# Kernel tuning notes

Hardware: AMD Instinct MI355X
Metric: run time of the kernel (lower is better)

Reference implementation:

```python
import jax, jax.numpy as jnp
import numpy as np

EPS = 1e-5


def layernorm(h, w, b):
    mu = jnp.mean(h, axis=-1, keepdims=True)
    var = jnp.mean((h - mu) ** 2, axis=-1, keepdims=True)
    return (h - mu) * jax.lax.rsqrt(var + EPS) * w + b


def pos_encoding(length, d_model):
    # PE(pos,2i)=sin(pos/10000^(2i/d)), PE(pos,2i+1)=cos(...)
    pos = jnp.arange(length, dtype=jnp.float32)[:, None]
    div = jnp.exp(jnp.arange(0, d_model, 2, dtype=jnp.float32) * (-np.log(10000.0) / d_model))
    pe = jnp.zeros((length, d_model), dtype=jnp.float32)
    pe = pe.at[:, 0::2].set(jnp.sin(pos * div))
    pe = pe.at[:, 1::2].set(jnp.cos(pos * div))
    return pe


def setup_inputs() -> dict:
    key = jax.random.key(0)
    ks = jax.random.split(key, 4)
    B, N, K, S = 4, 256, 128, 256
    return {
        "x": jax.random.normal(ks[0], (B, N, K, S), dtype=jnp.float32),
        "ln1_w": jnp.ones((N,), jnp.float32),
        "ln1_b": jnp.zeros((N,), jnp.float32),
        "q_w": jax.random.normal(ks[1], (N, N), jnp.float32) * 0.02,
        "q_b": jnp.zeros((N,), jnp.float32),
        "k_w": jax.random.normal(ks[2], (N, N), jnp.float32) * 0.02,
        "k_b": jnp.zeros((N,), jnp.float32),
        "v_w": jax.random.normal(ks[3], (N, N), jnp.float32) * 0.02,
        "v_b": jnp.zeros((N,), jnp.float32),
        "ln2_w": jnp.ones((N,), jnp.float32),
        "ln2_b": jnp.zeros((N,), jnp.float32),
    }


def reference(x, ln1_w, ln1_b, q_w, q_b, k_w, k_b, v_w, v_b, ln2_w, ln2_b):
    B, N, K, S = x.shape
    scale = 1.0 / np.sqrt(N)  # dim_k == in_channels
    # (B, N, K, S) -> (B*K, S, N)
    h = x.transpose(0, 2, 3, 1).reshape(B * K, S, N)
    h = layernorm(h, ln1_w, ln1_b) + pos_encoding(S, N)[None]
    res = h
    Q = h @ q_w.T + q_b
    Kt = h @ k_w.T + k_b
    V = h @ v_w.T + v_b
    # Faithful to source: softmax FIRST, then multiply by 1/sqrt(dim_k)
    att = jax.nn.softmax(jnp.einsum('bqd,bkd->bqk', Q, Kt), axis=-1) * scale
    h = res + jnp.einsum('bqk,bkd->bqd', att, V)  # dropout = identity (eval)
    h = layernorm(h, ln2_w, ln2_b)
    return h.reshape(B, K, S, N).transpose(0, 3, 1, 2) + x
```

## Files before the change

### kernel.cpp

```cpp
#include <hip/hip_runtime.h>


using short8  = __attribute__((ext_vector_type(8))) short;
using floatx4 = __attribute__((ext_vector_type(4))) float;

#define KSX 32768

__device__ __forceinline__ ushort f2bf(float f) {
    uint u = __float_as_uint(f);
    u += 0x7fffu + ((u >> 16) & 1u);
    return (ushort)(u >> 16);
}
__device__ __forceinline__ float bf2f(ushort h) {
    return __uint_as_float(((uint)h) << 16);
}

__global__ __launch_bounds__(256) void prep_kernel(
    const float* __restrict__ qw, const float* __restrict__ kw,
    const float* __restrict__ vw,
    float* __restrict__ pe, ushort* __restrict__ wpack)
{
    int tid = blockIdx.x * 256 + threadIdx.x;
    if (tid < 65536) {
        int n = tid >> 8, s = tid & 255;
        float d = expf(-0.03597789207803196f * (float)(n & ~1));
        float a = d * (float)s;
        pe[tid] = (n & 1) ? cosf(a) : sinf(a);
    } else {
        int id = tid - 65536;
        int wsel = id >> 16;
        int e = id & 65535;
        const float* w = (wsel == 0) ? qw : ((wsel == 1) ? kw : vw);
        int j    = e & 7;
        int lane = (e >> 3) & 63;
        int fr   = e >> 9;
        int nt   = fr & 15;
        int mc   = fr >> 4;
        int row  = (lane & 15) + 16 * nt;
        int col  = 8 * (lane >> 4) + j + 32 * mc;
        wpack[wsel * 65536 + e] = f2bf(w[row * 256 + col]);
    }
}

__global__ __launch_bounds__(512, 2) void attn_kernel(
    const float* __restrict__ x,
    const float* __restrict__ ln1w, const float* __restrict__ ln1b,
    const float* __restrict__ qbias, const float* __restrict__ kbias,
    const float* __restrict__ vbias,
    const float* __restrict__ ln2w, const float* __restrict__ ln2b,
    const float* __restrict__ pe, const ushort* __restrict__ wpack,
    float* __restrict__ out)
{
    __shared__ ushort ldsA[128 * 256];
    __shared__ ushort ldsB[128 * 256];
    __shared__ ushort bounce[8 * 512];
    __shared__ float  smallbuf[1792];
    __shared__ float  stats[512];

    const int tid = threadIdx.x;
    const int wid = tid >> 6;
    const int l   = tid & 63;
    const int c   = l & 15;
    const int g   = l >> 4;

    const int bk   = blockIdx.x;
    const int base = (bk >> 7) * (256 * KSX) + (bk & 127) * 256;
    const float* xb = x + base;
    float* ob = out + base;

    const short8* wq8 = (const short8*)(wpack);
    const short8* wk8 = (const short8*)(wpack + 65536);
    const short8* wv8 = (const short8*)(wpack + 131072);

    {
        int i = tid;
        smallbuf[i] = (i < 256) ? ln1w[i] : ln1b[i - 256];
        i = tid + 512;
        smallbuf[i] = (i < 768) ? ln2w[i - 512] : ln2b[i - 768];
        i = tid + 1024;
        smallbuf[i] = (i < 1280) ? qbias[i - 1024] : kbias[i - 1280];
        if (tid < 256) smallbuf[tid + 1536] = vbias[tid];
    }
    __syncthreads();

    ushort* bnc = bounce + (wid << 9);

    short8 Hfrag[2][8];
    #pragma unroll
    for (int t = 0; t < 2; ++t) {
        const int s = 16 * wid + 128 * t + c;
        float sum = 0.f, ssq = 0.f;
        #pragma unroll
        for (int mc = 0; mc < 8; ++mc) {
            short8 hp;
            #pragma unroll
            for (int j = 0; j < 8; ++j) {
                int m = 32 * mc + 8 * g + j;
                float v = xb[m * KSX + s];
                ushort hb = f2bf(v);
                hp[j] = (short)hb;
                float vb = bf2f(hb);
                sum += vb; ssq += vb * vb;
            }
            Hfrag[t][mc] = hp;
        }
        sum += __shfl_xor(sum, 16); ssq += __shfl_xor(ssq, 16);
        sum += __shfl_xor(sum, 32); ssq += __shfl_xor(ssq, 32);
        float mu   = sum * (1.f / 256.f);
        float var  = ssq * (1.f / 256.f) - mu * mu;
        float rstd = rsqrtf(var + 1e-5f);
        #pragma unroll
        for (int mc = 0; mc < 8; ++mc) {
            short8 hp = Hfrag[t][mc];
            #pragma unroll
            for (int j = 0; j < 8; ++j) {
                int m = 32 * mc + 8 * g + j;
                float v = bf2f((ushort)hp[j]);
                float h = (v - mu) * rstd * smallbuf[m] + smallbuf[256 + m]
                          + pe[m * 256 + s];
                hp[j] = (short)f2bf(h);
            }
            Hfrag[t][mc] = hp;
        }
        if (g == 0) { stats[2 * s] = mu; stats[2 * s + 1] = rstd; }
    }

    short8 Qfrag[2][8];
    #pragma unroll
    for (int t = 0; t < 2; ++t) {
        #pragma unroll
        for (int nc = 0; nc < 8; ++nc) {
            floatx4 acc0 = {0.f, 0.f, 0.f, 0.f};
            floatx4 acc1 = {0.f, 0.f, 0.f, 0.f};
            #pragma unroll
            for (int mc = 0; mc < 8; ++mc) {
                short8 a  = Hfrag[t][mc];
                short8 b0 = wq8[(mc * 16 + 2 * nc) * 64 + l];
                short8 b1 = wq8[(mc * 16 + 2 * nc + 1) * 64 + l];
                acc0 = __builtin_amdgcn_mfma_f32_16x16x32_bf16(a, b0, acc0, 0, 0, 0);
                acc1 = __builtin_amdgcn_mfma_f32_16x16x32_bf16(a, b1, acc1, 0, 0, 0);
            }
            #pragma unroll
            for (int e = 0; e < 2; ++e) {
                floatx4 acc = e ? acc1 : acc0;
                float bias = smallbuf[1024 + 16 * (2 * nc + e) + c];
                #pragma unroll
                for (int r = 0; r < 4; ++r) {
                    int row = 4 * g + r;
                    int col = 16 * e + c;
                    bnc[row * 32 + (col ^ ((row & 3) << 3))] = f2bf(acc[r] + bias);
                }
            }
            Qfrag[t][nc] = *(const short8*)&bnc[c * 32 + ((8 * g) ^ ((c & 3) << 3))];
        }
    }

    #pragma unroll
    for (int hf = 0; hf < 2; ++hf) {
        ushort* reg = hf ? ldsB : ldsA;
        #pragma unroll
        for (int nt = 0; nt < 16; ++nt) {
            floatx4 acc = {0.f, 0.f, 0.f, 0.f};
            #pragma unroll
            for (int mc = 0; mc < 8; ++mc)
                acc = __builtin_amdgcn_mfma_f32_16x16x32_bf16(
                    Hfrag[hf][mc], wk8[(mc * 16 + nt) * 64 + l], acc, 0, 0, 0);
            int n = 16 * nt + c;
            float bias = smallbuf[1280 + n];
            #pragma unroll
            for (int r = 0; r < 4; ++r) {
                int kkl = 16 * wid + 4 * g + r;
                reg[kkl * 256 + (n ^ ((kkl & 7) << 3))] = f2bf(acc[r] + bias);
            }
        }
    }
    __syncthreads();

    uint  Spack[2][4][8];
    float mloc[8];
    #pragma unroll
    for (int i = 0; i < 8; ++i) mloc[i] = -3.0e38f;

    #pragma unroll
    for (int ct = 0; ct < 16; ++ct) {
        const ushort* reg = (ct < 8) ? ldsA : ldsB;
        int kt = ct & 7;
        short8 bfr[8];
        #pragma unroll
        for (int mt = 0; mt < 8; ++mt) {
            int kkl = c + 16 * kt;
            int n0  = 32 * mt + 8 * g;
            bfr[mt] = *(const short8*)&reg[kkl * 256 + (n0 ^ ((kkl & 7) << 3))];
        }
        #pragma unroll
        for (int t = 0; t < 2; ++t) {
            floatx4 acc = {0.f, 0.f, 0.f, 0.f};
            #pragma unroll
            for (int mt = 0; mt < 8; ++mt)
                acc = __builtin_amdgcn_mfma_f32_16x16x32_bf16(
                    Qfrag[t][mt], bfr[mt], acc, 0, 0, 0);
            #pragma unroll
            for (int r = 0; r < 4; ++r) {
                float v = acc[r];
                mloc[t * 4 + r] = fmaxf(mloc[t * 4 + r], v);
                ushort hb = f2bf(v);
                if (ct & 1)
                    Spack[t][r][ct >> 1] = (Spack[t][r][ct >> 1] & 0xffffu) | ((uint)hb << 16);
                else
                    Spack[t][r][ct >> 1] = hb;
            }
        }
    }

    #pragma unroll
    for (int i = 0; i < 8; ++i) {
        mloc[i] = fmaxf(mloc[i], __shfl_xor(mloc[i], 1));
        mloc[i] = fmaxf(mloc[i], __shfl_xor(mloc[i], 2));
        mloc[i] = fmaxf(mloc[i], __shfl_xor(mloc[i], 4));
        mloc[i] = fmaxf(mloc[i], __shfl_xor(mloc[i], 8));
    }
    float lsum[8];
    #pragma unroll
    for (int i = 0; i < 8; ++i) lsum[i] = 0.f;
    #pragma unroll
    for (int t = 0; t < 2; ++t) {
        #pragma unroll
        for (int r = 0; r < 4; ++r) {
            float m = mloc[t * 4 + r];
            #pragma unroll
            for (int d0 = 0; d0 < 8; ++d0) {
                uint d = Spack[t][r][d0];
                float e0 = __expf(bf2f((ushort)(d & 0xffffu)) - m);
                float e1 = __expf(bf2f((ushort)(d >> 16)) - m);
                lsum[t * 4 + r] += e0 + e1;
                Spack[t][r][d0] = (uint)f2bf(e0) | ((uint)f2bf(e1) << 16);
            }
        }
    }
    #pragma unroll
    for (int i = 0; i < 8; ++i) {
        lsum[i] += __shfl_xor(lsum[i], 1);
        lsum[i] += __shfl_xor(lsum[i], 2);
        lsum[i] += __shfl_xor(lsum[i], 4);
        lsum[i] += __shfl_xor(lsum[i], 8);
    }

    short8 Pfrag[2][8];
    #pragma unroll
    for (int t = 0; t < 2; ++t) {
        #pragma unroll
        for (int kc = 0; kc < 8; ++kc) {
            #pragma unroll
            for (int r = 0; r < 4; ++r) {
                float f = 0.0625f / lsum[t * 4 + r];
                uint d = Spack[t][r][kc];
                int row = 4 * g + r;
                bnc[row * 32 + (c        ^ ((row & 3) << 3))] = f2bf(bf2f((ushort)(d & 0xffffu)) * f);
                bnc[row * 32 + ((16 + c) ^ ((row & 3) << 3))] = f2bf(bf2f((ushort)(d >> 16)) * f);
            }
            Pfrag[t][kc] = *(const short8*)&bnc[c * 32 + ((8 * g) ^ ((c & 3) << 3))];
        }
    }
    __syncthreads();

    #pragma unroll
    for (int hf = 0; hf < 2; ++hf) {
        ushort* reg = hf ? ldsB : ldsA;
        #pragma unroll
        for (int nt = 0; nt < 16; ++nt) {
            floatx4 acc = {0.f, 0.f, 0.f, 0.f};
            #pragma unroll
            for (int mc = 0; mc < 8; ++mc)
                acc = __builtin_amdgcn_mfma_f32_16x16x32_bf16(
                    Hfrag[hf][mc], wv8[(mc * 16 + nt) * 64 + l], acc, 0, 0, 0);
            int n = 16 * nt + c;
            float bias = smallbuf[1536 + n];
            #pragma unroll
            for (int r = 0; r < 4; ++r) {
                int kkl = 16 * wid + 4 * g + r;
                reg[n * 128 + (kkl ^ ((n & 7) << 3))] = f2bf(acc[r] + bias);
            }
        }
    }
    __syncthreads();

    floatx4 O[2][16];
    #pragma unroll
    for (int t = 0; t < 2; ++t)
        #pragma unroll
        for (int nt = 0; nt < 16; ++nt) {
            floatx4 z = {0.f, 0.f, 0.f, 0.f};
            O[t][nt] = z;
        }
    #pragma unroll
    for (int kc = 0; kc < 8; ++kc) {
        const ushort* reg = (kc < 4) ? ldsA : ldsB;
        int kc4 = kc & 3;
        #pragma unroll
        for (int nt = 0; nt < 16; ++nt) {
            int n  = c + 16 * nt;
            int k0 = 8 * g + 32 * kc4;
            short8 a = *(const short8*)&reg[n * 128 + (k0 ^ ((n & 7) << 3))];
            O[0][nt] = __builtin_amdgcn_mfma_f32_16x16x32_bf16(a, Pfrag[0][kc], O[0][nt], 0, 0, 0);
            O[1][nt] = __builtin_amdgcn_mfma_f32_16x16x32_bf16(a, Pfrag[1][kc], O[1][nt], 0, 0, 0);
        }
    }

    #pragma unroll
    for (int t = 0; t < 2; ++t) {
        const int q = 16 * wid + 128 * t + c;
        float mu1 = stats[2 * q], rstd1 = stats[2 * q + 1];
        float s1 = 0.f, s2 = 0.f;
        #pragma unroll
        for (int nt = 0; nt < 16; ++nt) {
            floatx4 o = O[t][nt];
            #pragma unroll
            for (int r = 0; r < 4; ++r) {
                int n = 16 * nt + 4 * g + r;
                float xv  = xb[n * KSX + q];
                float res = (xv - mu1) * rstd1 * smallbuf[n] + smallbuf[256 + n]
                            + pe[n * 256 + q];
                float h2 = res + o[r];
                o[r] = h2;
                s1 += h2; s2 += h2 * h2;
            }
            O[t][nt] = o;
        }
        s1 += __shfl_xor(s1, 16); s2 += __shfl_xor(s2, 16);
        s1 += __shfl_xor(s1, 32); s2 += __shfl_xor(s2, 32);
        float mu2   = s1 * (1.f / 256.f);
        float var2  = s2 * (1.f / 256.f) - mu2 * mu2;
        float rstd2 = rsqrtf(var2 + 1e-5f);
        #pragma unroll
        for (int nt = 0; nt < 16; ++nt) {
            floatx4 o = O[t][nt];
            #pragma unroll
            for (int r = 0; r < 4; ++r) {
                int n = 16 * nt + 4 * g + r;
                float xv = xb[n * KSX + q];
                float y  = (o[r] - mu2) * rstd2 * smallbuf[512 + n]
                           + smallbuf[768 + n] + xv;
                ob[n * KSX + q] = y;
            }
        }
    }
}

extern "C" void kernel_launch(void* const* d_in, const int* in_sizes, int n_in,
                              void* d_out, int out_size, void* d_ws, size_t ws_size,
                              hipStream_t stream)
{
    (void)in_sizes; (void)n_in; (void)out_size; (void)ws_size;
    const float* x    = (const float*)d_in[0];
    const float* ln1w = (const float*)d_in[1];
    const float* ln1b = (const float*)d_in[2];
    const float* qw   = (const float*)d_in[3];
    const float* qb   = (const float*)d_in[4];
    const float* kw   = (const float*)d_in[5];
    const float* kb   = (const float*)d_in[6];
    const float* vw   = (const float*)d_in[7];
    const float* vb   = (const float*)d_in[8];
    const float* ln2w = (const float*)d_in[9];
    const float* ln2b = (const float*)d_in[10];
    float* out = (float*)d_out;

    float*  pe    = (float*)d_ws;
    ushort* wpack = (ushort*)((char*)d_ws + 262144);

    prep_kernel<<<1024, 256, 0, stream>>>(qw, kw, vw, pe, wpack);
    attn_kernel<<<512, 512, 0, stream>>>(x, ln1w, ln1b, qb, kb, vb,
                                         ln2w, ln2b, pe, wpack, out);
}
```

Measured before the change: 1.388 ms.

## Split each attention instance across two blocks by query half

Doubles the grid so each block handles only 128 query rows of a sequence while still computing K and V for all 256 positions. The per-thread Q, score, probability and output register arrays shrink by half, reducing register pressure and possible spills. In exchange, the LayerNorm1, K and V projections and the loads of x for them are done twice per sequence.

```diff
diff --git a/kernel.cpp b/kernel.cpp
--- a/kernel.cpp
+++ b/kernel.cpp
@@ -63,7 +63,8 @@
     const int c   = l & 15;
     const int g   = l >> 4;
 
-    const int bk   = blockIdx.x;
+    const int bk   = blockIdx.x >> 1;
+    const int half = blockIdx.x & 1;
     const int base = (bk >> 7) * (256 * KSX) + (bk & 127) * 256;
     const float* xb = x + base;
     float* ob = out + base;
@@ -88,7 +89,7 @@
     short8 Hfrag[2][8];
     #pragma unroll
     for (int t = 0; t < 2; ++t) {
-        const int s = 16 * wid + 128 * t + c;
+        const int s = 128 * (half ^ t) + 16 * wid + c;
         float sum = 0.f, ssq = 0.f;
         #pragma unroll
         for (int mc = 0; mc < 8; ++mc) {
@@ -125,46 +126,43 @@
         if (g == 0) { stats[2 * s] = mu; stats[2 * s + 1] = rstd; }
     }
 
-    short8 Qfrag[2][8];
+    short8 Qfrag[8];
+    #pragma unroll
+    for (int nc = 0; nc < 8; ++nc) {
+        floatx4 acc0 = {0.f, 0.f, 0.f, 0.f};
+        floatx4 acc1 = {0.f, 0.f, 0.f, 0.f};
+        #pragma unroll
+        for (int mc = 0; mc < 8; ++mc) {
+            short8 a  = Hfrag[0][mc];
+            short8 b0 = wq8[(mc * 16 + 2 * nc) * 64 + l];
+            short8 b1 = wq8[(mc * 16 + 2 * nc + 1) * 64 + l];
+            acc0 = __builtin_amdgcn_mfma_f32_16x16x32_bf16(a, b0, acc0, 0, 0, 0);
+            acc1 = __builtin_amdgcn_mfma_f32_16x16x32_bf16(a, b1, acc1, 0, 0, 0);
+        }
+        #pragma unroll
+        for (int e = 0; e < 2; ++e) {
+            floatx4 acc = e ? acc1 : acc0;
+            float bias = smallbuf[1024 + 16 * (2 * nc + e) + c];
+            #pragma unroll
+            for (int r = 0; r < 4; ++r) {
+                int row = 4 * g + r;
+                int col = 16 * e + c;
+                bnc[row * 32 + (col ^ ((row & 3) << 3))] = f2bf(acc[r] + bias);
+            }
+        }
+        Qfrag[nc] = *(const short8*)&bnc[c * 32 + ((8 * g) ^ ((c & 3) << 3))];
+    }
+
     #pragma unroll
     for (int t = 0; t < 2; ++t) {
-        #pragma unroll
-        for (int nc = 0; nc < 8; ++nc) {
-            floatx4 acc0 = {0.f, 0.f, 0.f, 0.f};
-            floatx4 acc1 = {0.f, 0.f, 0.f, 0.f};
-            #pragma unroll
-            for (int mc = 0; mc < 8; ++mc) {
-                short8 a  = Hfrag[t][mc];
-                short8 b0 = wq8[(mc * 16 + 2 * nc) * 64 + l];
-                short8 b1 = wq8[(mc * 16 + 2 * nc + 1) * 64 + l];
-                acc0 = __builtin_amdgcn_mfma_f32_16x16x32_bf16(a, b0, acc0, 0, 0, 0);
-                acc1 = __builtin_amdgcn_mfma_f32_16x16x32_bf16(a, b1, acc1, 0, 0, 0);
-            }
-            #pragma unroll
-            for (int e = 0; e < 2; ++e) {
-                floatx4 acc = e ? acc1 : acc0;
-                float bias = smallbuf[1024 + 16 * (2 * nc + e) + c];
-                #pragma unroll
-                for (int r = 0; r < 4; ++r) {
-                    int row = 4 * g + r;
-                    int col = 16 * e + c;
-                    bnc[row * 32 + (col ^ ((row & 3) << 3))] = f2bf(acc[r] + bias);
-                }
-            }
-            Qfrag[t][nc] = *(const short8*)&bnc[c * 32 + ((8 * g) ^ ((c & 3) << 3))];
-        }
-    }
-
-    #pragma unroll
-    for (int hf = 0; hf < 2; ++hf) {
-        ushort* reg = hf ? ldsB : ldsA;
+        ushort* reg = (half ^ t) ? ldsB : ldsA;
         #pragma unroll
         for (int nt = 0; nt < 16; ++nt) {
             floatx4 acc = {0.f, 0.f, 0.f, 0.f};
             #pragma unroll
             for (int mc = 0; mc < 8; ++mc)
                 acc = __builtin_amdgcn_mfma_f32_16x16x32_bf16(
-                    Hfrag[hf][mc], wk8[(mc * 16 + nt) * 64 + l], acc, 0, 0, 0);
+                    Hfrag[t][mc], wk8[(mc * 16 + nt) * 64 + l], acc, 0, 0, 0);
             int n = 16 * nt + c;
             float bias = smallbuf[1280 + n];
             #pragma unroll
@@ -176,10 +174,10 @@
     }
     __syncthreads();
 
-    uint  Spack[2][4][8];
-    float mloc[8];
-    #pragma unroll
-    for (int i = 0; i < 8; ++i) mloc[i] = -3.0e38f;
+    uint  Spack[4][8];
+    float mloc[4];
+    #pragma unroll
+    for (int i = 0; i < 4; ++i) mloc[i] = -3.0e38f;
 
     #pragma unroll
     for (int ct = 0; ct < 16; ++ct) {
@@ -192,87 +190,78 @@
             int n0  = 32 * mt + 8 * g;
             bfr[mt] = *(const short8*)&reg[kkl * 256 + (n0 ^ ((kkl & 7) << 3))];
         }
-        #pragma unroll
-        for (int t = 0; t < 2; ++t) {
-            floatx4 acc = {0.f, 0.f, 0.f, 0.f};
-            #pragma unroll
-            for (int mt = 0; mt < 8; ++mt)
-                acc = __builtin_amdgcn_mfma_f32_16x16x32_bf16(
-                    Qfrag[t][mt], bfr[mt], acc, 0, 0, 0);
-            #pragma unroll
-            for (int r = 0; r < 4; ++r) {
-                float v = acc[r];
-                mloc[t * 4 + r] = fmaxf(mloc[t * 4 + r], v);
-                ushort hb = f2bf(v);
-                if (ct & 1)
-                    Spack[t][r][ct >> 1] = (Spack[t][r][ct >> 1] & 0xffffu) | ((uint)hb << 16);
-                else
-                    Spack[t][r][ct >> 1] = hb;
-            }
-        }
-    }
-
-    #pragma unroll
-    for (int i = 0; i < 8; ++i) {
+        floatx4 acc = {0.f, 0.f, 0.f, 0.f};
+        #pragma unroll
+        for (int mt = 0; mt < 8; ++mt)
+            acc = __builtin_amdgcn_mfma_f32_16x16x32_bf16(
+                Qfrag[mt], bfr[mt], acc, 0, 0, 0);
+        #pragma unroll
+        for (int r = 0; r < 4; ++r) {
+            float v = acc[r];
+            mloc[r] = fmaxf(mloc[r], v);
+            ushort hb = f2bf(v);
+            if (ct & 1)
+                Spack[r][ct >> 1] = (Spack[r][ct >> 1] & 0xffffu) | ((uint)hb << 16);
+            else
+                Spack[r][ct >> 1] = hb;
+        }
+    }
+
+    #pragma unroll
+    for (int i = 0; i < 4; ++i) {
         mloc[i] = fmaxf(mloc[i], __shfl_xor(mloc[i], 1));
         mloc[i] = fmaxf(mloc[i], __shfl_xor(mloc[i], 2));
         mloc[i] = fmaxf(mloc[i], __shfl_xor(mloc[i], 4));
         mloc[i] = fmaxf(mloc[i], __shfl_xor(mloc[i], 8));
     }
-    float lsum[8];
-    #pragma unroll
-    for (int i = 0; i < 8; ++i) lsum[i] = 0.f;
-    #pragma unroll
-    for (int t = 0; t < 2; ++t) {
-        #pragma unroll
-        for (int r = 0; r < 4; ++r) {
-            float m = mloc[t * 4 + r];
-            #pragma unroll
-            for (int d0 = 0; d0 < 8; ++d0) {
-                uint d = Spack[t][r][d0];
-                float e0 = __expf(bf2f((ushort)(d & 0xffffu)) - m);
-                float e1 = __expf(bf2f((ushort)(d >> 16)) - m);
-                lsum[t * 4 + r] += e0 + e1;
-                Spack[t][r][d0] = (uint)f2bf(e0) | ((uint)f2bf(e1) << 16);
-            }
-        }
-    }
-    #pragma unroll
-    for (int i = 0; i < 8; ++i) {
+    float lsum[4];
+    #pragma unroll
+    for (int i = 0; i < 4; ++i) lsum[i] = 0.f;
+    #pragma unroll
+    for (int r = 0; r < 4; ++r) {
+        float m = mloc[r];
+        #pragma unroll
+        for (int d0 = 0; d0 < 8; ++d0) {
+            uint d = Spack[r][d0];
+            float e0 = __expf(bf2f((ushort)(d & 0xffffu)) - m);
+            float e1 = __expf(bf2f((ushort)(d >> 16)) - m);
+            lsum[r] += e0 + e1;
+            Spack[r][d0] = (uint)f2bf(e0) | ((uint)f2bf(e1) << 16);
+        }
+    }
+    #pragma unroll
+    for (int i = 0; i < 4; ++i) {
         lsum[i] += __shfl_xor(lsum[i], 1);
         lsum[i] += __shfl_xor(lsum[i], 2);
         lsum[i] += __shfl_xor(lsum[i], 4);
         lsum[i] += __shfl_xor(lsum[i], 8);
     }
 
-    short8 Pfrag[2][8];
+    short8 Pfrag[8];
+    #pragma unroll
+    for (int kc = 0; kc < 8; ++kc) {
+        #pragma unroll
+        for (int r = 0; r < 4; ++r) {
+            float f = 0.0625f / lsum[r];
+            uint d = Spack[r][kc];
+            int row = 4 * g + r;
+            bnc[row * 32 + (c        ^ ((row & 3) << 3))] = f2bf(bf2f((ushort)(d & 0xffffu)) * f);
+            bnc[row * 32 + ((16 + c) ^ ((row & 3) << 3))] = f2bf(bf2f((ushort)(d >> 16)) * f);
+        }
+        Pfrag[kc] = *(const short8*)&bnc[c * 32 + ((8 * g) ^ ((c & 3) << 3))];
+    }
+    __syncthreads();
+
     #pragma unroll
     for (int t = 0; t < 2; ++t) {
-        #pragma unroll
-        for (int kc = 0; kc < 8; ++kc) {
-            #pragma unroll
-            for (int r = 0; r < 4; ++r) {
-                float f = 0.0625f / lsum[t * 4 + r];
-                uint d = Spack[t][r][kc];
-                int row = 4 * g + r;
-                bnc[row * 32 + (c        ^ ((row & 3) << 3))] = f2bf(bf2f((ushort)(d & 0xffffu)) * f);
-                bnc[row * 32 + ((16 + c) ^ ((row & 3) << 3))] = f2bf(bf2f((ushort)(d >> 16)) * f);
-            }
-            Pfrag[t][kc] = *(const short8*)&bnc[c * 32 + ((8 * g) ^ ((c & 3) << 3))];
-        }
-    }
-    __syncthreads();
-
-    #pragma unroll
-    for (int hf = 0; hf < 2; ++hf) {
-        ushort* reg = hf ? ldsB : ldsA;
+        ushort* reg = (half ^ t) ? ldsB : ldsA;
         #pragma unroll
         for (int nt = 0; nt < 16; ++nt) {
             floatx4 acc = {0.f, 0.f, 0.f, 0.f};
             #pragma unroll
             for (int mc = 0; mc < 8; ++mc)
                 acc = __builtin_amdgcn_mfma_f32_16x16x32_bf16(
-                    Hfrag[hf][mc], wv8[(mc * 16 + nt) * 64 + l], acc, 0, 0, 0);
+                    Hfrag[t][mc], wv8[(mc * 16 + nt) * 64 + l], acc, 0, 0, 0);
             int n = 16 * nt + c;
             float bias = smallbuf[1536 + n];
             #pragma unroll
@@ -284,14 +273,12 @@
     }
     __syncthreads();
 
-    floatx4 O[2][16];
-    #pragma unroll
-    for (int t = 0; t < 2; ++t)
-        #pragma unroll
-        for (int nt = 0; nt < 16; ++nt) {
-            floatx4 z = {0.f, 0.f, 0.f, 0.f};
-            O[t][nt] = z;
-        }
+    floatx4 O[16];
+    #pragma unroll
+    for (int nt = 0; nt < 16; ++nt) {
+        floatx4 z = {0.f, 0.f, 0.f, 0.f};
+        O[nt] = z;
+    }
     #pragma unroll
     for (int kc = 0; kc < 8; ++kc) {
         const ushort* reg = (kc < 4) ? ldsA : ldsB;
@@ -301,19 +288,17 @@
             int n  = c + 16 * nt;
             int k0 = 8 * g + 32 * kc4;
             short8 a = *(const short8*)&reg[n * 128 + (k0 ^ ((n & 7) << 3))];
-            O[0][nt] = __builtin_amdgcn_mfma_f32_16x16x32_bf16(a, Pfrag[0][kc], O[0][nt], 0, 0, 0);
-            O[1][nt] = __builtin_amdgcn_mfma_f32_16x16x32_bf16(a, Pfrag[1][kc], O[1][nt], 0, 0, 0);
-        }
-    }
-
-    #pragma unroll
-    for (int t = 0; t < 2; ++t) {
-        const int q = 16 * wid + 128 * t + c;
+            O[nt] = __builtin_amdgcn_mfma_f32_16x16x32_bf16(a, Pfrag[kc], O[nt], 0, 0, 0);
+        }
+    }
+
+    {
+        const int q = 128 * half + 16 * wid + c;
         float mu1 = stats[2 * q], rstd1 = stats[2 * q + 1];
         float s1 = 0.f, s2 = 0.f;
         #pragma unroll
         for (int nt = 0; nt < 16; ++nt) {
-            floatx4 o = O[t][nt];
+            floatx4 o = O[nt];
             #pragma unroll
             for (int r = 0; r < 4; ++r) {
                 int n = 16 * nt + 4 * g + r;
@@ -324,7 +309,7 @@
                 o[r] = h2;
                 s1 += h2; s2 += h2 * h2;
             }
-            O[t][nt] = o;
+            O[nt] = o;
         }
         s1 += __shfl_xor(s1, 16); s2 += __shfl_xor(s2, 16);
         s1 += __shfl_xor(s1, 32); s2 += __shfl_xor(s2, 32);
@@ -333,7 +318,7 @@
         float rstd2 = rsqrtf(var2 + 1e-5f);
         #pragma unroll
         for (int nt = 0; nt < 16; ++nt) {
-            floatx4 o = O[t][nt];
+            floatx4 o = O[nt];
             #pragma unroll
             for (int r = 0; r < 4; ++r) {
                 int n = 16 * nt + 4 * g + r;
@@ -368,6 +353,6 @@
     ushort* wpack = (ushort*)((char*)d_ws + 262144);
 
     prep_kernel<<<1024, 256, 0, stream>>>(qw, kw, vw, pe, wpack);
-    attn_kernel<<<512, 512, 0, stream>>>(x, ln1w, ln1b, qb, kb, vb,
-                                         ln2w, ln2b, pe, wpack, out);
-}
+    attn_kernel<<<1024, 512, 0, stream>>>(x, ln1w, ln1b, qb, kb, vb,
+                                          ln2w, ln2b, pe, wpack, out);
+}
```

Measured after the change: 1.538 ms. 1.11x slower.
